# Kernel tuning notes

Hardware: AMD Instinct MI355X
Metric: run time of the kernel (lower is better)

The kernel has to match this reference:

```python
import jax, jax.numpy as jnp
import numpy as np

B, S, N, F = 4, 256, 128, 64
D = 128          # d_model == 2*F so encoder/decoder dims agree
NH = 4           # hard-coded num_heads in both MHA blocks


def _linear(x, w, b):
    # torch nn.Linear: y = x @ W.T + b, W: (out, in)
    return x @ w.T + b


def _mha(q, k, v, w_in, b_in, w_out, b_out, nh):
    # torch nn.MultiheadAttention (batch_first=True) with packed in_proj
    bq, sq, e = q.shape
    hd = e // nh
    qp = _linear(q, w_in[:e], b_in[:e])
    kp = _linear(k, w_in[e:2 * e], b_in[e:2 * e])
    vp = _linear(v, w_in[2 * e:], b_in[2 * e:])
    qh = qp.reshape(bq, sq, nh, hd)
    kh = kp.reshape(bq, k.shape[1], nh, hd)
    vh = vp.reshape(bq, v.shape[1], nh, hd)
    scores = jnp.einsum('bqhd,bkhd->bhqk', qh, kh) / np.sqrt(hd).astype(np.float32)
    attn = jax.nn.softmax(scores, axis=-1)
    out = jnp.einsum('bhqk,bkhd->bqhd', attn, vh).reshape(bq, sq, e)
    return _linear(out, w_out, b_out)


def _pos_enc(s, d):
    pos = jnp.arange(s, dtype=jnp.float32)[:, None]
    div = jnp.exp(jnp.arange(0, d, 2, dtype=jnp.float32) * (-np.log(10000.0) / d))
    pe = jnp.zeros((s, d), dtype=jnp.float32)
    pe = pe.at[:, 0::2].set(jnp.sin(pos * div))
    pe = pe.at[:, 1::2].set(jnp.cos(pos * div))
    return pe


def _haar_decouple(x):
    # exact vectorized pywt haar dwt + single-branch idwt (even seq_len)
    b, s, n, f = x.shape
    pairs = x.reshape(b, s // 2, 2, n, f)
    avg = (pairs[:, :, 0] + pairs[:, :, 1]) * 0.5  # idwt(cA, None) value
    dif = (pairs[:, :, 0] - pairs[:, :, 1]) * 0.5  # idwt(None, cD) value
    x_l = jnp.stack([avg, avg], axis=2).reshape(b, s, n, f)
    x_h = jnp.stack([dif, -dif], axis=2).reshape(b, s, n, f)
    return x_l, x_h


def setup_inputs() -> dict:
    key = jax.random.key(0)
    ks = jax.random.split(key, 32)
    p = lambda i, shp: jax.random.normal(ks[i], shp, jnp.float32) * 0.02
    return {
        'x': jax.random.normal(ks[0], (B, S, N, F), jnp.float32),
        'ts': jax.random.randint(ks[1], (B, S), 0, 252),
        'ta_w_in': p(2, (3 * D, D)), 'ta_b_in': p(3, (3 * D,)),
        'ta_w_out': p(4, (D, D)), 'ta_b_out': p(5, (D,)),
        'conv_w': p(6, (D, 2 * F, 3)), 'conv_b': p(7, (D,)),
        'pl_w': p(8, (D, D)), 'pl_b': p(9, (D,)),
        'ph_w': p(10, (D, D)), 'ph_b': p(11, (D,)),
        'as_w_in': p(12, (3 * D, D)), 'as_b_in': p(13, (3 * D,)),
        'as_w_out': p(14, (D, D)), 'as_b_out': p(15, (D,)),
        'ac_w_in': p(16, (3 * D, D)), 'ac_b_in': p(17, (3 * D,)),
        'ac_w_out': p(18, (D, D)), 'ac_b_out': p(19, (D,)),
        'rl_w': p(20, (1, D)), 'rl_b': p(21, (1,)),
        'cl_w': p(22, (2, D)), 'cl_b': p(23, (2,)),
        'rf_w': p(24, (1, D)), 'rf_b': p(25, (1,)),
        'cf_w': p(26, (2, D)), 'cf_b': p(27, (2,)),
    }


def reference(x, ts, ta_w_in, ta_b_in, ta_w_out, ta_b_out, conv_w, conv_b,
              pl_w, pl_b, ph_w, ph_b, as_w_in, as_b_in, as_w_out, as_b_out,
              ac_w_in, ac_b_in, ac_w_out, ac_b_out, rl_w, rl_b, cl_w, cl_b,
              rf_w, rf_b, cf_w, cf_b):
    b, s, n, f = x.shape
    # --- DecouplingFlowLayer (vectorized haar) ---
    x_l, x_h = _haar_decouple(x)
    xl_cat = jnp.concatenate([x, x_l], axis=-1)  # (b,s,n,2f)
    xh_cat = jnp.concatenate([x, x_h], axis=-1)
    e = 2 * f
    # --- DualFrequencyEncoder ---
    pe = _pos_enc(s, e)
    xl_flat = xl_cat.transpose(0, 2, 1, 3).reshape(b * n, s, e) + pe
    x_tatt = _mha(xl_flat, xl_flat, xl_flat, ta_w_in, ta_b_in, ta_w_out, ta_b_out, NH)
    x_l_gat = x_tatt.reshape(b, s, n, e)  # faithful raw .view() as in torch
    xh_flat = xh_cat.transpose(0, 2, 3, 1).reshape(b * n, e, s)
    conv = jax.lax.conv_general_dilated(
        xh_flat, conv_w, window_strides=(1,), padding=[(2, 2)],
        rhs_dilation=(2,), dimension_numbers=('NCH', 'OIH', 'NCH'))
    conv = jax.nn.relu(conv + conv_b[None, :, None])
    x_h_gat = conv.reshape(b, n, -1, s).transpose(0, 3, 1, 2)  # (b,s,n,D)
    d = x_h_gat.shape[-1]
    # ts -> time_embedding is computed then discarded in the original forward: dead code
    # --- DualFrequencyFusionDecoder ---
    y_l = x_l_gat.reshape(b * n, s, d)
    y_h = x_h_gat.reshape(b * n, s, d)
    q_l = _linear(y_l, pl_w, pl_b)
    k_h = _linear(y_h, ph_w, ph_b)
    y_l2 = _linear(q_l, pl_w, pl_b)  # predictor_l applied twice, as in torch
    lreg = _linear(y_l2, rl_w, rl_b).reshape(b, s, n)
    lcla = jax.nn.softmax(_linear(y_l2, cl_w, cl_b), axis=-1).reshape(b, s, n, 2)
    a_self = _mha(q_l, q_l, q_l, as_w_in, as_b_in, as_w_out, as_b_out, NH)
    a_cross = _mha(q_l, k_h, k_h, ac_w_in, ac_b_in, ac_w_out, ac_b_out, NH)
    fused = (a_self + a_cross).reshape(b, s, n, d)
    reg = _linear(fused, rf_w, rf_b)[..., 0]
    cla = jax.nn.softmax(_linear(fused, cf_w, cf_b), axis=-1)
    return reg, cla, lreg, lcla
```

## Files before the change

kernel.cpp:

```cpp
#include <hip/hip_runtime.h>
#include <hip/hip_bf16.h>

typedef __attribute__((ext_vector_type(8))) short short8v;
typedef __attribute__((ext_vector_type(4))) short short4v;
typedef __attribute__((ext_vector_type(4))) float f32x4;
typedef __hip_bfloat16 bh;

constexpr long SF_ELEMS = 131072L * 128;
#define MFMA16(a, b, c) __builtin_amdgcn_mfma_f32_16x16x32_bf16((a), (b), (c), 0, 0, 0)

__device__ __forceinline__ short bh_bits(float x) {
  bh h = __float2bfloat16(x);
  return *reinterpret_cast<short*>(&h);
}


__global__ __launch_bounds__(256) void sf_wcvt(const float* __restrict__ s0, const float* __restrict__ s1,
                                               const float* __restrict__ s2, const float* __restrict__ s3,
                                               const float* __restrict__ s4, const float* __restrict__ s5,
                                               const float* __restrict__ s6, const float* __restrict__ s7,
                                               const float* __restrict__ cw,
                                               bh* __restrict__ dst) {
  int i = blockIdx.x * 256 + threadIdx.x;
  float v;
  if      (i <  49152) v = s0[i];
  else if (i <  65536) v = s1[i - 49152];
  else if (i <  81920) v = s2[i - 65536];
  else if (i <  98304) v = s3[i - 81920];
  else if (i < 147456) v = s4[i - 98304];
  else if (i < 163840) v = s5[i - 147456];
  else if (i < 212992) v = s6[i - 163840];
  else if (i < 229376) v = s7[i - 212992];
  else if (i < 278528) {
    int j = i - 229376;
    int tap = j >> 14, rem = j & 16383;
    v = cw[rem * 3 + tap];
  } else return;
  dst[i] = __float2bfloat16(v);
}

__global__ __launch_bounds__(256) void sf_pe(float* __restrict__ pe) {
  int i = blockIdx.x * 256 + threadIdx.x;
  int e = i & 127, s = i >> 7;
  int ii = e >> 1;
  float dv = expf(-0.0719557945041855f * (float)(2 * ii));
  float ang = (float)s * dv;
  pe[i] = (e & 1) ? cosf(ang) : sinf(ang);
}

__global__ __launch_bounds__(256) void sf_buildzx(const float* __restrict__ x,
                                                  const float* __restrict__ pe,
                                                  bh* __restrict__ z,
                                                  bh* __restrict__ xh) {
  long i = (long)blockIdx.x * 256 + threadIdx.x;
  if (i >= SF_ELEMS) return;
  int e = (int)(i & 127);
  int s = (int)((i >> 7) & 255);
  int r = (int)(i >> 15);
  int b = r >> 7, stk = r & 127;
  float zv, hv;
  if (e < 64) {
    float val = x[(((long)b * 256 + s) * 128 + stk) * 64 + e];
    zv = val; hv = val;
  } else {
    int f = e - 64;
    int t2 = s >> 1;
    float a0 = x[(((long)b * 256 + 2 * t2) * 128 + stk) * 64 + f];
    float a1 = x[(((long)b * 256 + 2 * t2 + 1) * 128 + stk) * 64 + f];
    zv = 0.5f * (a0 + a1);
    float d = 0.5f * (a0 - a1);
    hv = (s & 1) ? -d : d;
  }
  z[i] = __float2bfloat16(zv + pe[s * 128 + e]);
  xh[i] = __float2bfloat16(hv);
}

__global__ __launch_bounds__(256) void sf_lin(const bh* __restrict__ X,
                                              const bh* __restrict__ Wb,
                                              const float* __restrict__ bias,
                                              bh* __restrict__ Y) {
  __shared__ bh Lw[4][32][140];
  const int t = threadIdx.x, lane = t & 63, w = t >> 6;
  const int lr = lane & 15, lg = lane >> 4;
  const long R0 = (long)blockIdx.x * 128 + w * 32;
  const f32x4 z4 = {0.f, 0.f, 0.f, 0.f};
  short8v a[2][4];
#pragma unroll
  for (int ks = 0; ks < 4; ++ks) {
    a[0][ks] = *reinterpret_cast<const short8v*>(X + (R0 + lr) * 128 + ks * 32 + lg * 8);
    a[1][ks] = *reinterpret_cast<const short8v*>(X + (R0 + 16 + lr) * 128 + ks * 32 + lg * 8);
  }
  f32x4 acc[2][8];
#pragma unroll
  for (int m = 0; m < 2; ++m)
#pragma unroll
    for (int n = 0; n < 8; ++n) acc[m][n] = z4;
#pragma unroll
  for (int ks = 0; ks < 4; ++ks) {
#pragma unroll
    for (int n = 0; n < 8; ++n) {
      short8v b = *reinterpret_cast<const short8v*>(Wb + (long)(n * 16 + lr) * 128 + ks * 32 + lg * 8);
      acc[0][n] = MFMA16(a[0][ks], b, acc[0][n]);
      acc[1][n] = MFMA16(a[1][ks], b, acc[1][n]);
    }
  }
#pragma unroll
  for (int n = 0; n < 8; ++n) {
    float bv = bias[n * 16 + lr];
#pragma unroll
    for (int m = 0; m < 2; ++m)
#pragma unroll
      for (int r = 0; r < 4; ++r)
        Lw[w][m * 16 + 4 * lg + r][n * 16 + lr] = __float2bfloat16(acc[m][n][r] + bv);
  }
#pragma unroll
  for (int c = 0; c < 8; ++c) {
    int row_l = c * 4 + lg;
    short8v v = *reinterpret_cast<const short8v*>(&Lw[w][row_l][lr * 8]);
    *reinterpret_cast<short8v*>(Y + (R0 + row_l) * 128 + lr * 8) = v;
  }
}

__global__ __launch_bounds__(256) void sf_convm(const bh* __restrict__ Xh,
                                                const bh* __restrict__ Wr,
                                                const float* __restrict__ bias,
                                                bh* __restrict__ Yh) {
  __shared__ bh Lw[4][32][140];
  const int t = threadIdx.x, lane = t & 63, w = t >> 6;
  const int lr = lane & 15, lg = lane >> 4;
  const int bnc = blockIdx.x >> 1;
  const int half = blockIdx.x & 1;
  const int b = bnc >> 7, stk = bnc & 127;
  const int R0 = half * 128 + w * 32;
  const f32x4 z4 = {0.f, 0.f, 0.f, 0.f};
  const short8v zf = {0, 0, 0, 0, 0, 0, 0, 0};
  f32x4 acc[2][8];
#pragma unroll
  for (int m = 0; m < 2; ++m)
#pragma unroll
    for (int n = 0; n < 8; ++n) acc[m][n] = z4;
#pragma unroll
  for (int tap = 0; tap < 3; ++tap) {
    const int shift = 2 * tap - 2;
#pragma unroll
    for (int ks = 0; ks < 4; ++ks) {
      int s0 = R0 + lr + shift;
      int s1 = s0 + 16;
      short8v a0 = zf, a1 = zf;
      if ((unsigned)s0 < 256u)
        a0 = *reinterpret_cast<const short8v*>(Xh + ((long)bnc * 256 + s0) * 128 + ks * 32 + lg * 8);
      if ((unsigned)s1 < 256u)
        a1 = *reinterpret_cast<const short8v*>(Xh + ((long)bnc * 256 + s1) * 128 + ks * 32 + lg * 8);
#pragma unroll
      for (int n = 0; n < 8; ++n) {
        short8v bb = *reinterpret_cast<const short8v*>(Wr + (long)tap * 16384 + (long)(n * 16 + lr) * 128 + ks * 32 + lg * 8);
        acc[0][n] = MFMA16(a0, bb, acc[0][n]);
        acc[1][n] = MFMA16(a1, bb, acc[1][n]);
      }
    }
  }
#pragma unroll
  for (int n = 0; n < 8; ++n) {
    float bv = bias[n * 16 + lr];
#pragma unroll
    for (int m = 0; m < 2; ++m)
#pragma unroll
      for (int r = 0; r < 4; ++r)
        Lw[w][m * 16 + 4 * lg + r][n * 16 + lr] = __float2bfloat16(fmaxf(acc[m][n][r] + bv, 0.f));
  }
#pragma unroll
  for (int c = 0; c < 8; ++c) {
    int row_l = c * 4 + lg;
    int sc = R0 + row_l;
    int rp = b * 128 + (sc >> 1);
    int sp = ((sc & 1) << 7) + stk;
    short8v v = *reinterpret_cast<const short8v*>(&Lw[w][row_l][lr * 8]);
    *reinterpret_cast<short8v*>(Yh + ((long)rp * 256 + sp) * 128 + lr * 8) = v;
  }
}

__global__ __launch_bounds__(256) void sf_attnp(const bh* Qsrc, const bh* KVsrc,
                                                const bh* __restrict__ Win,
                                                const float* __restrict__ bin,
                                                bh* __restrict__ O) {
  __shared__ bh Ks[256][36];
  __shared__ bh Vt[32][260];
  __shared__ bh QP[4][64][36];
  const int t = threadIdx.x, lane = t & 63, w = t >> 6;
  const int lr = lane & 15, lg = lane >> 4;
  const int bn = blockIdx.x >> 2, h = blockIdx.x & 3;
  const long R0 = (long)bn * 256;
  const int ch = h * 32;
  const f32x4 z4 = {0.f, 0.f, 0.f, 0.f};
  const float SC2 = 0.2550351f;
  {
    short8v wq[2][4];
#pragma unroll
    for (int n = 0; n < 2; ++n)
#pragma unroll
      for (int ks = 0; ks < 4; ++ks)
        wq[n][ks] = *reinterpret_cast<const short8v*>(Win + (long)(ch + n * 16 + lr) * 128 + ks * 32 + lg * 8);
#pragma unroll
    for (int m2 = 0; m2 < 4; ++m2) {
      short8v asv[4];
#pragma unroll
      for (int ks = 0; ks < 4; ++ks)
        asv[ks] = *reinterpret_cast<const short8v*>(Qsrc + (R0 + w * 64 + m2 * 16 + lr) * 128 + ks * 32 + lg * 8);
#pragma unroll
      for (int n = 0; n < 2; ++n) {
        f32x4 acc = z4;
#pragma unroll
        for (int ks = 0; ks < 4; ++ks) acc = MFMA16(asv[ks], wq[n][ks], acc);
        float bb = bin[ch + n * 16 + lr];
#pragma unroll
        for (int r = 0; r < 4; ++r)
          QP[w][m2 * 16 + 4 * lg + r][n * 16 + lr] = __float2bfloat16((acc[r] + bb) * SC2);
      }
    }
  }
  {
    short8v wk[2][4], wv[2][4];
#pragma unroll
    for (int n = 0; n < 2; ++n)
#pragma unroll
      for (int ks = 0; ks < 4; ++ks) {
        wk[n][ks] = *reinterpret_cast<const short8v*>(Win + (long)(128 + ch + n * 16 + lr) * 128 + ks * 32 + lg * 8);
        wv[n][ks] = *reinterpret_cast<const short8v*>(Win + (long)(256 + ch + n * 16 + lr) * 128 + ks * 32 + lg * 8);
      }
#pragma unroll
    for (int m2 = 0; m2 < 4; ++m2) {
      short8v asv[4];
#pragma unroll
      for (int ks = 0; ks < 4; ++ks)
        asv[ks] = *reinterpret_cast<const short8v*>(KVsrc + (R0 + w * 64 + m2 * 16 + lr) * 128 + ks * 32 + lg * 8);
#pragma unroll
      for (int n = 0; n < 2; ++n) {
        f32x4 ak = z4, av = z4;
#pragma unroll
        for (int ks = 0; ks < 4; ++ks) {
          ak = MFMA16(asv[ks], wk[n][ks], ak);
          av = MFMA16(asv[ks], wv[n][ks], av);
        }
        float bk = bin[128 + ch + n * 16 + lr];
        float bv = bin[256 + ch + n * 16 + lr];
#pragma unroll
        for (int r = 0; r < 4; ++r)
          Ks[w * 64 + m2 * 16 + 4 * lg + r][n * 16 + lr] = __float2bfloat16(ak[r] + bk);
        short4v pv;
#pragma unroll
        for (int r = 0; r < 4; ++r) pv[r] = bh_bits(av[r] + bv);
        *reinterpret_cast<short4v*>(&Vt[n * 16 + lr][w * 64 + m2 * 16 + 4 * lg]) = pv;
      }
    }
  }
  __syncthreads();
  short8v aq[4];
#pragma unroll
  for (int mt = 0; mt < 4; ++mt)
    aq[mt] = *reinterpret_cast<const short8v*>(&QP[w][mt * 16 + lr][lg * 8]);
  bh* plp = &QP[w][0][0];
  f32x4 Oacc[4][2];
  float psum[4] = {0.f, 0.f, 0.f, 0.f};
#pragma unroll
  for (int mt = 0; mt < 4; ++mt) { Oacc[mt][0] = z4; Oacc[mt][1] = z4; }
#pragma unroll
  for (int kt = 0; kt < 4; ++kt) {
    short8v bvf[2][2];
#pragma unroll
    for (int dt = 0; dt < 2; ++dt)
#pragma unroll
      for (int ks = 0; ks < 2; ++ks)
        bvf[dt][ks] = *reinterpret_cast<const short8v*>(&Vt[dt * 16 + lr][kt * 64 + ks * 32 + lg * 8]);
#pragma unroll
    for (int mt = 0; mt < 4; ++mt) {
      f32x4 st[4];
#pragma unroll
      for (int nt = 0; nt < 4; ++nt) {
        short8v bk = *reinterpret_cast<const short8v*>(&Ks[kt * 64 + nt * 16 + lr][lg * 8]);
        st[nt] = MFMA16(bk, aq[mt], z4);
      }
      float ps = 0.f;
#pragma unroll
      for (int nt = 0; nt < 4; ++nt) {
        float p0 = exp2f(st[nt][0]);
        float p1 = exp2f(st[nt][1]);
        float p2 = exp2f(st[nt][2]);
        float p3 = exp2f(st[nt][3]);
        ps += (p0 + p1) + (p2 + p3);
        short4v pk;
        pk[0] = bh_bits(p0); pk[1] = bh_bits(p1); pk[2] = bh_bits(p2); pk[3] = bh_bits(p3);
        *reinterpret_cast<short4v*>(&plp[lr * 72 + nt * 16 + 4 * lg]) = pk;
      }
      psum[mt] += ps;
#pragma unroll
      for (int ks = 0; ks < 2; ++ks) {
        short8v ap = *reinterpret_cast<const short8v*>(&plp[lr * 72 + ks * 32 + lg * 8]);
        Oacc[mt][0] = MFMA16(ap, bvf[0][ks], Oacc[mt][0]);
        Oacc[mt][1] = MFMA16(ap, bvf[1][ks], Oacc[mt][1]);
      }
    }
  }
#pragma unroll
  for (int mt = 0; mt < 4; ++mt) {
    float ps = psum[mt];
    ps += __shfl_xor(ps, 16, 64);
    ps += __shfl_xor(ps, 32, 64);
    float inv = 1.f / ps;
#pragma unroll
    for (int r = 0; r < 4; ++r) {
      float invr = __shfl(inv, 4 * lg + r, 64);
      long row = R0 + w * 64 + mt * 16 + 4 * lg + r;
      O[row * 128 + ch + lr]      = __float2bfloat16(Oacc[mt][0][r] * invr);
      O[row * 128 + ch + 16 + lr] = __float2bfloat16(Oacc[mt][1][r] * invr);
    }
  }
}

__global__ __launch_bounds__(256) void sf_encdec(const bh* __restrict__ X,
                                                 const bh* __restrict__ Wo, const float* __restrict__ bo,
                                                 const bh* __restrict__ Wpl, const float* __restrict__ bpl,
                                                 const float* __restrict__ rw, const float* __restrict__ rb,
                                                 const float* __restrict__ cw, const float* __restrict__ cb,
                                                 bh* __restrict__ Yq, float* __restrict__ out,
                                                 long off_reg, long off_cla) {
  __shared__ bh Lw[4][32][140];
  __shared__ float hw[3][128];
  const int t = threadIdx.x, lane = t & 63, w = t >> 6;
  const int lr = lane & 15, lg = lane >> 4;
  const long R0 = (long)blockIdx.x * 128 + w * 32;
  const f32x4 z4 = {0.f, 0.f, 0.f, 0.f};
  if (t < 128) { hw[0][t] = rw[t]; hw[1][t] = cw[t]; hw[2][t] = cw[128 + t]; }
  {
    short8v a[2][4];
#pragma unroll
    for (int ks = 0; ks < 4; ++ks) {
      a[0][ks] = *reinterpret_cast<const short8v*>(X + (R0 + lr) * 128 + ks * 32 + lg * 8);
      a[1][ks] = *reinterpret_cast<const short8v*>(X + (R0 + 16 + lr) * 128 + ks * 32 + lg * 8);
    }
    f32x4 acc[2][8];
#pragma unroll
    for (int m = 0; m < 2; ++m)
#pragma unroll
      for (int n = 0; n < 8; ++n) acc[m][n] = z4;
#pragma unroll
    for (int ks = 0; ks < 4; ++ks)
#pragma unroll
      for (int n = 0; n < 8; ++n) {
        short8v b = *reinterpret_cast<const short8v*>(Wo + (long)(n * 16 + lr) * 128 + ks * 32 + lg * 8);
        acc[0][n] = MFMA16(a[0][ks], b, acc[0][n]);
        acc[1][n] = MFMA16(a[1][ks], b, acc[1][n]);
      }
#pragma unroll
    for (int n = 0; n < 8; ++n) {
      float bv = bo[n * 16 + lr];
#pragma unroll
      for (int m = 0; m < 2; ++m)
#pragma unroll
        for (int r = 0; r < 4; ++r)
          Lw[w][m * 16 + 4 * lg + r][n * 16 + lr] = __float2bfloat16(acc[m][n][r] + bv);
    }
  }
#pragma unroll
  for (int stage = 0; stage < 2; ++stage) {
    short8v a[2][4];
#pragma unroll
    for (int ks = 0; ks < 4; ++ks) {
      a[0][ks] = *reinterpret_cast<const short8v*>(&Lw[w][lr][ks * 32 + lg * 8]);
      a[1][ks] = *reinterpret_cast<const short8v*>(&Lw[w][16 + lr][ks * 32 + lg * 8]);
    }
    f32x4 acc[2][8];
#pragma unroll
    for (int m = 0; m < 2; ++m)
#pragma unroll
      for (int n = 0; n < 8; ++n) acc[m][n] = z4;
#pragma unroll
    for (int ks = 0; ks < 4; ++ks)
#pragma unroll
      for (int n = 0; n < 8; ++n) {
        short8v b = *reinterpret_cast<const short8v*>(Wpl + (long)(n * 16 + lr) * 128 + ks * 32 + lg * 8);
        acc[0][n] = MFMA16(a[0][ks], b, acc[0][n]);
        acc[1][n] = MFMA16(a[1][ks], b, acc[1][n]);
      }
#pragma unroll
    for (int n = 0; n < 8; ++n) {
      float bv = bpl[n * 16 + lr];
#pragma unroll
      for (int m = 0; m < 2; ++m)
#pragma unroll
        for (int r = 0; r < 4; ++r)
          Lw[w][m * 16 + 4 * lg + r][n * 16 + lr] = __float2bfloat16(acc[m][n][r] + bv);
    }
    if (stage == 0) {
#pragma unroll
      for (int c = 0; c < 8; ++c) {
        int row_l = c * 4 + lg;
        short8v v = *reinterpret_cast<const short8v*>(&Lw[w][row_l][lr * 8]);
        *reinterpret_cast<short8v*>(Yq + (R0 + row_l) * 128 + lr * 8) = v;
      }
    }
  }
  __syncthreads();
  {
    const int rr = lane >> 1, hh = lane & 1;
    float d0 = 0.f, d1 = 0.f, d2 = 0.f;
#pragma unroll
    for (int j = 0; j < 8; ++j) {
      short8v v8 = *reinterpret_cast<const short8v*>(&Lw[w][rr][hh * 64 + j * 8]);
      const bh* vv = reinterpret_cast<const bh*>(&v8);
#pragma unroll
      for (int k = 0; k < 8; ++k) {
        float f = __bfloat162float(vv[k]);
        int c = hh * 64 + j * 8 + k;
        d0 = fmaf(f, hw[0][c], d0);
        d1 = fmaf(f, hw[1][c], d1);
        d2 = fmaf(f, hw[2][c], d2);
      }
    }
    d0 += __shfl_xor(d0, 1, 64);
    d1 += __shfl_xor(d1, 1, 64);
    d2 += __shfl_xor(d2, 1, 64);
    if (hh == 0) {
      long row = R0 + rr;
      d0 += rb[0]; d1 += cb[0]; d2 += cb[1];
      float mx = fmaxf(d1, d2);
      float e1 = __expf(d1 - mx), e2 = __expf(d2 - mx);
      float inv = 1.f / (e1 + e2);
      out[off_reg + row] = d0;
      out[off_cla + row * 2] = e1 * inv;
      out[off_cla + row * 2 + 1] = e2 * inv;
    }
  }
}

__global__ __launch_bounds__(256) void sf_fin(const bh* __restrict__ X,
                                              const bh* __restrict__ Was, const float* __restrict__ bo,
                                              const bh* __restrict__ Prev,
                                              const float* __restrict__ rw, const float* __restrict__ rb,
                                              const float* __restrict__ cw, const float* __restrict__ cb,
                                              float* __restrict__ out, long off_reg, long off_cla) {
  __shared__ bh Lw[4][32][140];
  __shared__ float hw[3][128];
  const int t = threadIdx.x, lane = t & 63, w = t >> 6;
  const int lr = lane & 15, lg = lane >> 4;
  const long R0 = (long)blockIdx.x * 128 + w * 32;
  const f32x4 z4 = {0.f, 0.f, 0.f, 0.f};
  if (t < 128) { hw[0][t] = rw[t]; hw[1][t] = cw[t]; hw[2][t] = cw[128 + t]; }
  {
    short8v a[2][4];
#pragma unroll
    for (int ks = 0; ks < 4; ++ks) {
      a[0][ks] = *reinterpret_cast<const short8v*>(X + (R0 + lr) * 128 + ks * 32 + lg * 8);
      a[1][ks] = *reinterpret_cast<const short8v*>(X + (R0 + 16 + lr) * 128 + ks * 32 + lg * 8);
    }
    f32x4 acc[2][8];
#pragma unroll
    for (int m = 0; m < 2; ++m)
#pragma unroll
      for (int n = 0; n < 8; ++n) acc[m][n] = z4;
#pragma unroll
    for (int ks = 0; ks < 4; ++ks)
#pragma unroll
      for (int n = 0; n < 8; ++n) {
        short8v b = *reinterpret_cast<const short8v*>(Was + (long)(n * 16 + lr) * 128 + ks * 32 + lg * 8);
        acc[0][n] = MFMA16(a[0][ks], b, acc[0][n]);
        acc[1][n] = MFMA16(a[1][ks], b, acc[1][n]);
      }
#pragma unroll
    for (int n = 0; n < 8; ++n) {
      float bv = bo[n * 16 + lr];
#pragma unroll
      for (int m = 0; m < 2; ++m)
#pragma unroll
        for (int r = 0; r < 4; ++r)
          Lw[w][m * 16 + 4 * lg + r][n * 16 + lr] = __float2bfloat16(acc[m][n][r] + bv);
    }
  }
  __syncthreads();
  {
    const int rr = lane >> 1, hh = lane & 1;
    float d0 = 0.f, d1 = 0.f, d2 = 0.f;
#pragma unroll
    for (int j = 0; j < 8; ++j) {
      short8v v8 = *reinterpret_cast<const short8v*>(&Lw[w][rr][hh * 64 + j * 8]);
      short8v p8 = *reinterpret_cast<const short8v*>(Prev + (R0 + rr) * 128 + hh * 64 + j * 8);
      const bh* vv = reinterpret_cast<const bh*>(&v8);
      const bh* pp = reinterpret_cast<const bh*>(&p8);
#pragma unroll
      for (int k = 0; k < 8; ++k) {
        float f = __bfloat162float(vv[k]) + __bfloat162float(pp[k]);
        int c = hh * 64 + j * 8 + k;
        d0 = fmaf(f, hw[0][c], d0);
        d1 = fmaf(f, hw[1][c], d1);
        d2 = fmaf(f, hw[2][c], d2);
      }
    }
    d0 += __shfl_xor(d0, 1, 64);
    d1 += __shfl_xor(d1, 1, 64);
    d2 += __shfl_xor(d2, 1, 64);
    if (hh == 0) {
      long row = R0 + rr;
      d0 += rb[0]; d1 += cb[0]; d2 += cb[1];
      float mx = fmaxf(d1, d2);
      float e1 = __expf(d1 - mx), e2 = __expf(d2 - mx);
      float inv = 1.f / (e1 + e2);
      out[off_reg + row] = d0;
      out[off_cla + row * 2] = e1 * inv;
      out[off_cla + row * 2 + 1] = e2 * inv;
    }
  }
}

extern "C" void kernel_launch(void* const* d_in, const int* in_sizes, int n_in,
                              void* d_out, int out_size, void* d_ws, size_t ws_size,
                              hipStream_t stream) {
  (void)in_sizes; (void)n_in; (void)out_size; (void)ws_size;
  const float* x       = (const float*)d_in[0];
  const float* ta_w_in = (const float*)d_in[2];
  const float* ta_b_in = (const float*)d_in[3];
  const float* ta_w_o  = (const float*)d_in[4];
  const float* ta_b_o  = (const float*)d_in[5];
  const float* conv_w  = (const float*)d_in[6];
  const float* conv_b  = (const float*)d_in[7];
  const float* pl_w    = (const float*)d_in[8];
  const float* pl_b    = (const float*)d_in[9];
  const float* ph_w    = (const float*)d_in[10];
  const float* ph_b    = (const float*)d_in[11];
  const float* as_w_in = (const float*)d_in[12];
  const float* as_b_in = (const float*)d_in[13];
  const float* as_w_o  = (const float*)d_in[14];
  const float* as_b_o  = (const float*)d_in[15];
  const float* ac_w_in = (const float*)d_in[16];
  const float* ac_b_in = (const float*)d_in[17];
  const float* ac_w_o  = (const float*)d_in[18];
  const float* ac_b_o  = (const float*)d_in[19];
  const float* rl_w    = (const float*)d_in[20];
  const float* rl_b    = (const float*)d_in[21];
  const float* cl_w    = (const float*)d_in[22];
  const float* cl_b    = (const float*)d_in[23];
  const float* rf_w    = (const float*)d_in[24];
  const float* rf_b    = (const float*)d_in[25];
  const float* cf_w    = (const float*)d_in[26];
  const float* cf_b    = (const float*)d_in[27];
  float* out = (float*)d_out;

  bh* S0 = (bh*)d_ws;
  bh* S1 = S0 + SF_ELEMS;
  bh* S2 = S1 + SF_ELEMS;
  bh* S3 = S2 + SF_ELEMS;
  bh* S4 = S3 + SF_ELEMS;
  bh* A  = S4 + SF_ELEMS;
  float* PE = (float*)(A + 278528);

  dim3 blk(256);
  const int GZ = (int)(SF_ELEMS / 256);
  const int GL = 1024;

  sf_wcvt<<<1088, blk, 0, stream>>>(ta_w_in, ta_w_o, pl_w, ph_w, ac_w_in, ac_w_o,
                                    as_w_in, as_w_o, conv_w, A);
  sf_pe<<<128, blk, 0, stream>>>(PE);

  sf_buildzx<<<GZ, blk, 0, stream>>>(x, PE, S0, S3);
  sf_attnp<<<2048, blk, 0, stream>>>(S0, S0, A, ta_b_in, S1);
  sf_encdec<<<GL, blk, 0, stream>>>(S1, A + 49152, ta_b_o, A + 65536, pl_b,
                                    rl_w, rl_b, cl_w, cl_b, S2, out,
                                    393216L, 524288L);
  sf_convm<<<1024, blk, 0, stream>>>(S3, A + 229376, conv_b, S4);
  sf_lin<<<GL, blk, 0, stream>>>(S4, A + 81920, ph_b, S0);

  sf_attnp<<<2048, blk, 0, stream>>>(S2, S0, A + 98304, ac_b_in, S3);
  sf_lin<<<GL, blk, 0, stream>>>(S3, A + 147456, ac_b_o, S4);

  sf_attnp<<<2048, blk, 0, stream>>>(S2, S2, A + 163840, as_b_in, S1);
  sf_fin<<<GL, blk, 0, stream>>>(S1, A + 212992, as_b_o, S4,
                                 rf_w, rf_b, cf_w, cf_b, out, 0L, 131072L);
}
```

Before: 471.2 us.

## Merge independent decoder stages into combined launches and fuse output projections

Folds positional-encoding generation into the weight-conversion kernel. Runs the encoder-output/predictor chain and the conv+predictor_h chain in one launch, split by block index. Runs the cross- and self-attention kernels together in a single launch. Fuses both attention output projections into the final head kernel by summing the two GEMMs in one accumulator. The aim is fewer launches, fewer intermediate round trips through global memory, and better GPU fill; the cost is larger kernels that may use more registers, with uneven work across the blocks of a merged launch.

Measured after the change: 479.3 us. Within noise of the previous version (+1.7%).

```diff
diff --git a/kernel.cpp b/kernel.cpp
--- a/kernel.cpp
+++ b/kernel.cpp
@@ -20,8 +20,19 @@
                                                const float* __restrict__ s4, const float* __restrict__ s5,
                                                const float* __restrict__ s6, const float* __restrict__ s7,
                                                const float* __restrict__ cw,
-                                               bh* __restrict__ dst) {
+                                               bh* __restrict__ dst, float* __restrict__ pe) {
   int i = blockIdx.x * 256 + threadIdx.x;
+  if (i >= 278528) {
+    int j = i - 278528;
+    if (j < 32768) {
+      int e = j & 127, s = j >> 7;
+      int ii = e >> 1;
+      float dv = expf(-0.0719557945041855f * (float)(2 * ii));
+      float ang = (float)s * dv;
+      pe[j] = (e & 1) ? cosf(ang) : sinf(ang);
+    }
+    return;
+  }
   float v;
   if      (i <  49152) v = s0[i];
   else if (i <  65536) v = s1[i - 49152];
@@ -31,21 +42,12 @@
   else if (i < 163840) v = s5[i - 147456];
   else if (i < 212992) v = s6[i - 163840];
   else if (i < 229376) v = s7[i - 212992];
-  else if (i < 278528) {
+  else {
     int j = i - 229376;
     int tap = j >> 14, rem = j & 16383;
     v = cw[rem * 3 + tap];
-  } else return;
+  }
   dst[i] = __float2bfloat16(v);
-}
-
-__global__ __launch_bounds__(256) void sf_pe(float* __restrict__ pe) {
-  int i = blockIdx.x * 256 + threadIdx.x;
-  int e = i & 127, s = i >> 7;
-  int ii = e >> 1;
-  float dv = expf(-0.0719557945041855f * (float)(2 * ii));
-  float ang = (float)s * dv;
-  pe[i] = (e & 1) ? cosf(ang) : sinf(ang);
 }
 
 __global__ __launch_bounds__(256) void sf_buildzx(const float* __restrict__ x,
@@ -75,125 +77,21 @@
   xh[i] = __float2bfloat16(hv);
 }
 
-__global__ __launch_bounds__(256) void sf_lin(const bh* __restrict__ X,
-                                              const bh* __restrict__ Wb,
-                                              const float* __restrict__ bias,
-                                              bh* __restrict__ Y) {
-  __shared__ bh Lw[4][32][140];
+__device__ __forceinline__ void attn_body(const bh* Qsrc, const bh* KVsrc,
+                                          const bh* __restrict__ Win,
+                                          const float* __restrict__ bin,
+                                          bh* __restrict__ O, int bn, int h,
+                                          bh (*Ks)[36], bh (*Vt)[260],
+                                          bh (*Pl)[2][16][72]) {
   const int t = threadIdx.x, lane = t & 63, w = t >> 6;
   const int lr = lane & 15, lg = lane >> 4;
-  const long R0 = (long)blockIdx.x * 128 + w * 32;
-  const f32x4 z4 = {0.f, 0.f, 0.f, 0.f};
-  short8v a[2][4];
-#pragma unroll
-  for (int ks = 0; ks < 4; ++ks) {
-    a[0][ks] = *reinterpret_cast<const short8v*>(X + (R0 + lr) * 128 + ks * 32 + lg * 8);
-    a[1][ks] = *reinterpret_cast<const short8v*>(X + (R0 + 16 + lr) * 128 + ks * 32 + lg * 8);
-  }
-  f32x4 acc[2][8];
-#pragma unroll
-  for (int m = 0; m < 2; ++m)
-#pragma unroll
-    for (int n = 0; n < 8; ++n) acc[m][n] = z4;
-#pragma unroll
-  for (int ks = 0; ks < 4; ++ks) {
-#pragma unroll
-    for (int n = 0; n < 8; ++n) {
-      short8v b = *reinterpret_cast<const short8v*>(Wb + (long)(n * 16 + lr) * 128 + ks * 32 + lg * 8);
-      acc[0][n] = MFMA16(a[0][ks], b, acc[0][n]);
-      acc[1][n] = MFMA16(a[1][ks], b, acc[1][n]);
-    }
-  }
-#pragma unroll
-  for (int n = 0; n < 8; ++n) {
-    float bv = bias[n * 16 + lr];
-#pragma unroll
-    for (int m = 0; m < 2; ++m)
-#pragma unroll
-      for (int r = 0; r < 4; ++r)
-        Lw[w][m * 16 + 4 * lg + r][n * 16 + lr] = __float2bfloat16(acc[m][n][r] + bv);
-  }
-#pragma unroll
-  for (int c = 0; c < 8; ++c) {
-    int row_l = c * 4 + lg;
-    short8v v = *reinterpret_cast<const short8v*>(&Lw[w][row_l][lr * 8]);
-    *reinterpret_cast<short8v*>(Y + (R0 + row_l) * 128 + lr * 8) = v;
-  }
-}
-
-__global__ __launch_bounds__(256) void sf_convm(const bh* __restrict__ Xh,
-                                                const bh* __restrict__ Wr,
-                                                const float* __restrict__ bias,
-                                                bh* __restrict__ Yh) {
-  __shared__ bh Lw[4][32][140];
-  const int t = threadIdx.x, lane = t & 63, w = t >> 6;
-  const int lr = lane & 15, lg = lane >> 4;
-  const int bnc = blockIdx.x >> 1;
-  const int half = blockIdx.x & 1;
-  const int b = bnc >> 7, stk = bnc & 127;
-  const int R0 = half * 128 + w * 32;
-  const f32x4 z4 = {0.f, 0.f, 0.f, 0.f};
-  const short8v zf = {0, 0, 0, 0, 0, 0, 0, 0};
-  f32x4 acc[2][8];
-#pragma unroll
-  for (int m = 0; m < 2; ++m)
-#pragma unroll
-    for (int n = 0; n < 8; ++n) acc[m][n] = z4;
-#pragma unroll
-  for (int tap = 0; tap < 3; ++tap) {
-    const int shift = 2 * tap - 2;
-#pragma unroll
-    for (int ks = 0; ks < 4; ++ks) {
-      int s0 = R0 + lr + shift;
-      int s1 = s0 + 16;
-      short8v a0 = zf, a1 = zf;
-      if ((unsigned)s0 < 256u)
-        a0 = *reinterpret_cast<const short8v*>(Xh + ((long)bnc * 256 + s0) * 128 + ks * 32 + lg * 8);
-      if ((unsigned)s1 < 256u)
-        a1 = *reinterpret_cast<const short8v*>(Xh + ((long)bnc * 256 + s1) * 128 + ks * 32 + lg * 8);
-#pragma unroll
-      for (int n = 0; n < 8; ++n) {
-        short8v bb = *reinterpret_cast<const short8v*>(Wr + (long)tap * 16384 + (long)(n * 16 + lr) * 128 + ks * 32 + lg * 8);
-        acc[0][n] = MFMA16(a0, bb, acc[0][n]);
-        acc[1][n] = MFMA16(a1, bb, acc[1][n]);
-      }
-    }
-  }
-#pragma unroll
-  for (int n = 0; n < 8; ++n) {
-    float bv = bias[n * 16 + lr];
-#pragma unroll
-    for (int m = 0; m < 2; ++m)
-#pragma unroll
-      for (int r = 0; r < 4; ++r)
-        Lw[w][m * 16 + 4 * lg + r][n * 16 + lr] = __float2bfloat16(fmaxf(acc[m][n][r] + bv, 0.f));
-  }
-#pragma unroll
-  for (int c = 0; c < 8; ++c) {
-    int row_l = c * 4 + lg;
-    int sc = R0 + row_l;
-    int rp = b * 128 + (sc >> 1);
-    int sp = ((sc & 1) << 7) + stk;
-    short8v v = *reinterpret_cast<const short8v*>(&Lw[w][row_l][lr * 8]);
-    *reinterpret_cast<short8v*>(Yh + ((long)rp * 256 + sp) * 128 + lr * 8) = v;
-  }
-}
-
-__global__ __launch_bounds__(256) void sf_attnp(const bh* Qsrc, const bh* KVsrc,
-                                                const bh* __restrict__ Win,
-                                                const float* __restrict__ bin,
-                                                bh* __restrict__ O) {
-  __shared__ bh Ks[256][36];
-  __shared__ bh Vt[32][260];
-  __shared__ bh QP[4][64][36];
-  const int t = threadIdx.x, lane = t & 63, w = t >> 6;
-  const int lr = lane & 15, lg = lane >> 4;
-  const int bn = blockIdx.x >> 2, h = blockIdx.x & 3;
   const long R0 = (long)bn * 256;
   const int ch = h * 32;
   const f32x4 z4 = {0.f, 0.f, 0.f, 0.f};
   const float SC2 = 0.2550351f;
+  short8v aq[4];
   {
+    bh* scr = &Pl[w][0][0][0];
     short8v wq[2][4];
 #pragma unroll
     for (int n = 0; n < 2; ++n)
@@ -214,8 +112,9 @@
         float bb = bin[ch + n * 16 + lr];
 #pragma unroll
         for (int r = 0; r < 4; ++r)
-          QP[w][m2 * 16 + 4 * lg + r][n * 16 + lr] = __float2bfloat16((acc[r] + bb) * SC2);
-      }
+          scr[(4 * lg + r) * 72 + n * 16 + lr] = __float2bfloat16((acc[r] + bb) * SC2);
+      }
+      aq[m2] = *reinterpret_cast<const short8v*>(&scr[lr * 72 + lg * 8]);
     }
   }
   {
@@ -254,11 +153,6 @@
     }
   }
   __syncthreads();
-  short8v aq[4];
-#pragma unroll
-  for (int mt = 0; mt < 4; ++mt)
-    aq[mt] = *reinterpret_cast<const short8v*>(&QP[w][mt * 16 + lr][lg * 8]);
-  bh* plp = &QP[w][0][0];
   f32x4 Oacc[4][2];
   float psum[4] = {0.f, 0.f, 0.f, 0.f};
 #pragma unroll
@@ -273,6 +167,7 @@
         bvf[dt][ks] = *reinterpret_cast<const short8v*>(&Vt[dt * 16 + lr][kt * 64 + ks * 32 + lg * 8]);
 #pragma unroll
     for (int mt = 0; mt < 4; ++mt) {
+      bh* plp = &Pl[w][mt & 1][0][0];
       f32x4 st[4];
 #pragma unroll
       for (int nt = 0; nt < 4; ++nt) {
@@ -316,13 +211,243 @@
   }
 }
 
-__global__ __launch_bounds__(256) void sf_encdec(const bh* __restrict__ X,
-                                                 const bh* __restrict__ Wo, const float* __restrict__ bo,
-                                                 const bh* __restrict__ Wpl, const float* __restrict__ bpl,
-                                                 const float* __restrict__ rw, const float* __restrict__ rb,
-                                                 const float* __restrict__ cw, const float* __restrict__ cb,
-                                                 bh* __restrict__ Yq, float* __restrict__ out,
-                                                 long off_reg, long off_cla) {
+__global__ __launch_bounds__(256) void sf_attnp(const bh* Qsrc, const bh* KVsrc,
+                                                const bh* __restrict__ Win,
+                                                const float* __restrict__ bin,
+                                                bh* __restrict__ O) {
+  __shared__ bh Ks[256][36];
+  __shared__ bh Vt[32][260];
+  __shared__ bh Pl[4][2][16][72];
+  attn_body(Qsrc, KVsrc, Win, bin, O, blockIdx.x >> 2, blockIdx.x & 3, Ks, Vt, Pl);
+}
+
+__global__ __launch_bounds__(256) void sf_attnp2(const bh* Qc, const bh* KVc,
+                                                 const bh* __restrict__ Wc, const float* __restrict__ bc,
+                                                 bh* __restrict__ Oc,
+                                                 const bh* Qs, const bh* KVs,
+                                                 const bh* __restrict__ Wsl, const float* __restrict__ bsl,
+                                                 bh* __restrict__ Os) {
+  __shared__ bh Ks[256][36];
+  __shared__ bh Vt[32][260];
+  __shared__ bh Pl[4][2][16][72];
+  int g = blockIdx.x;
+  if (g < 2048)
+    attn_body(Qc, KVc, Wc, bc, Oc, g >> 2, g & 3, Ks, Vt, Pl);
+  else {
+    g -= 2048;
+    attn_body(Qs, KVs, Wsl, bsl, Os, g >> 2, g & 3, Ks, Vt, Pl);
+  }
+}
+
+__global__ __launch_bounds__(256) void sf_dec(const bh* __restrict__ X,
+                                              const bh* __restrict__ Wo, const float* __restrict__ bo,
+                                              const bh* __restrict__ Wpl, const float* __restrict__ bpl,
+                                              const float* __restrict__ rw, const float* __restrict__ rb,
+                                              const float* __restrict__ cw, const float* __restrict__ cb,
+                                              bh* __restrict__ Yq, float* __restrict__ out,
+                                              long off_reg, long off_cla,
+                                              const bh* __restrict__ Xh,
+                                              const bh* __restrict__ Wr, const float* __restrict__ cbias,
+                                              const bh* __restrict__ Wph, const float* __restrict__ bph,
+                                              bh* __restrict__ KH) {
+  __shared__ bh Lw[4][32][140];
+  __shared__ float hw[3][128];
+  const int t = threadIdx.x, lane = t & 63, w = t >> 6;
+  const int lr = lane & 15, lg = lane >> 4;
+  const f32x4 z4 = {0.f, 0.f, 0.f, 0.f};
+  if (blockIdx.x < 1024) {
+    const long R0 = (long)blockIdx.x * 128 + w * 32;
+    if (t < 128) { hw[0][t] = rw[t]; hw[1][t] = cw[t]; hw[2][t] = cw[128 + t]; }
+    {
+      short8v a[2][4];
+#pragma unroll
+      for (int ks = 0; ks < 4; ++ks) {
+        a[0][ks] = *reinterpret_cast<const short8v*>(X + (R0 + lr) * 128 + ks * 32 + lg * 8);
+        a[1][ks] = *reinterpret_cast<const short8v*>(X + (R0 + 16 + lr) * 128 + ks * 32 + lg * 8);
+      }
+      f32x4 acc[2][8];
+#pragma unroll
+      for (int m = 0; m < 2; ++m)
+#pragma unroll
+        for (int n = 0; n < 8; ++n) acc[m][n] = z4;
+#pragma unroll
+      for (int ks = 0; ks < 4; ++ks)
+#pragma unroll
+        for (int n = 0; n < 8; ++n) {
+          short8v b = *reinterpret_cast<const short8v*>(Wo + (long)(n * 16 + lr) * 128 + ks * 32 + lg * 8);
+          acc[0][n] = MFMA16(a[0][ks], b, acc[0][n]);
+          acc[1][n] = MFMA16(a[1][ks], b, acc[1][n]);
+        }
+#pragma unroll
+      for (int n = 0; n < 8; ++n) {
+        float bv = bo[n * 16 + lr];
+#pragma unroll
+        for (int m = 0; m < 2; ++m)
+#pragma unroll
+          for (int r = 0; r < 4; ++r)
+            Lw[w][m * 16 + 4 * lg + r][n * 16 + lr] = __float2bfloat16(acc[m][n][r] + bv);
+      }
+    }
+#pragma unroll
+    for (int stage = 0; stage < 2; ++stage) {
+      short8v a[2][4];
+#pragma unroll
+      for (int ks = 0; ks < 4; ++ks) {
+        a[0][ks] = *reinterpret_cast<const short8v*>(&Lw[w][lr][ks * 32 + lg * 8]);
+        a[1][ks] = *reinterpret_cast<const short8v*>(&Lw[w][16 + lr][ks * 32 + lg * 8]);
+      }
+      f32x4 acc[2][8];
+#pragma unroll
+      for (int m = 0; m < 2; ++m)
+#pragma unroll
+        for (int n = 0; n < 8; ++n) acc[m][n] = z4;
+#pragma unroll
+      for (int ks = 0; ks < 4; ++ks)
+#pragma unroll
+        for (int n = 0; n < 8; ++n) {
+          short8v b = *reinterpret_cast<const short8v*>(Wpl + (long)(n * 16 + lr) * 128 + ks * 32 + lg * 8);
+          acc[0][n] = MFMA16(a[0][ks], b, acc[0][n]);
+          acc[1][n] = MFMA16(a[1][ks], b, acc[1][n]);
+        }
+#pragma unroll
+      for (int n = 0; n < 8; ++n) {
+        float bv = bpl[n * 16 + lr];
+#pragma unroll
+        for (int m = 0; m < 2; ++m)
+#pragma unroll
+          for (int r = 0; r < 4; ++r)
+            Lw[w][m * 16 + 4 * lg + r][n * 16 + lr] = __float2bfloat16(acc[m][n][r] + bv);
+      }
+      if (stage == 0) {
+#pragma unroll
+        for (int c = 0; c < 8; ++c) {
+          int row_l = c * 4 + lg;
+          short8v v = *reinterpret_cast<const short8v*>(&Lw[w][row_l][lr * 8]);
+          *reinterpret_cast<short8v*>(Yq + (R0 + row_l) * 128 + lr * 8) = v;
+        }
+      }
+    }
+    __syncthreads();
+    {
+      const int rr = lane >> 1, hh = lane & 1;
+      float d0 = 0.f, d1 = 0.f, d2 = 0.f;
+#pragma unroll
+      for (int j = 0; j < 8; ++j) {
+        short8v v8 = *reinterpret_cast<const short8v*>(&Lw[w][rr][hh * 64 + j * 8]);
+        const bh* vv = reinterpret_cast<const bh*>(&v8);
+#pragma unroll
+        for (int k = 0; k < 8; ++k) {
+          float f = __bfloat162float(vv[k]);
+          int c = hh * 64 + j * 8 + k;
+          d0 = fmaf(f, hw[0][c], d0);
+          d1 = fmaf(f, hw[1][c], d1);
+          d2 = fmaf(f, hw[2][c], d2);
+        }
+      }
+      d0 += __shfl_xor(d0, 1, 64);
+      d1 += __shfl_xor(d1, 1, 64);
+      d2 += __shfl_xor(d2, 1, 64);
+      if (hh == 0) {
+        long row = R0 + rr;
+        d0 += rb[0]; d1 += cb[0]; d2 += cb[1];
+        float mx = fmaxf(d1, d2);
+        float e1 = __expf(d1 - mx), e2 = __expf(d2 - mx);
+        float inv = 1.f / (e1 + e2);
+        out[off_reg + row] = d0;
+        out[off_cla + row * 2] = e1 * inv;
+        out[off_cla + row * 2 + 1] = e2 * inv;
+      }
+    }
+  } else {
+    int bid = blockIdx.x - 1024;
+    const int bnc = bid >> 1;
+    const int half = bid & 1;
+    const int b = bnc >> 7, stk = bnc & 127;
+    const int R0 = half * 128 + w * 32;
+    const short8v zf = {0, 0, 0, 0, 0, 0, 0, 0};
+    f32x4 acc[2][8];
+#pragma unroll
+    for (int m = 0; m < 2; ++m)
+#pragma unroll
+      for (int n = 0; n < 8; ++n) acc[m][n] = z4;
+#pragma unroll
+    for (int tap = 0; tap < 3; ++tap) {
+      const int shift = 2 * tap - 2;
+#pragma unroll
+      for (int ks = 0; ks < 4; ++ks) {
+        int s0 = R0 + lr + shift;
+        int s1 = s0 + 16;
+        short8v a0 = zf, a1 = zf;
+        if ((unsigned)s0 < 256u)
+          a0 = *reinterpret_cast<const short8v*>(Xh + ((long)bnc * 256 + s0) * 128 + ks * 32 + lg * 8);
+        if ((unsigned)s1 < 256u)
+          a1 = *reinterpret_cast<const short8v*>(Xh + ((long)bnc * 256 + s1) * 128 + ks * 32 + lg * 8);
+#pragma unroll
+        for (int n = 0; n < 8; ++n) {
+          short8v bb = *reinterpret_cast<const short8v*>(Wr + (long)tap * 16384 + (long)(n * 16 + lr) * 128 + ks * 32 + lg * 8);
+          acc[0][n] = MFMA16(a0, bb, acc[0][n]);
+          acc[1][n] = MFMA16(a1, bb, acc[1][n]);
+        }
+      }
+    }
+#pragma unroll
+    for (int n = 0; n < 8; ++n) {
+      float bv = cbias[n * 16 + lr];
+#pragma unroll
+      for (int m = 0; m < 2; ++m)
+#pragma unroll
+        for (int r = 0; r < 4; ++r)
+          Lw[w][m * 16 + 4 * lg + r][n * 16 + lr] = __float2bfloat16(fmaxf(acc[m][n][r] + bv, 0.f));
+    }
+    {
+      short8v a2[2][4];
+#pragma unroll
+      for (int ks = 0; ks < 4; ++ks) {
+        a2[0][ks] = *reinterpret_cast<const short8v*>(&Lw[w][lr][ks * 32 + lg * 8]);
+        a2[1][ks] = *reinterpret_cast<const short8v*>(&Lw[w][16 + lr][ks * 32 + lg * 8]);
+      }
+      f32x4 ac2[2][8];
+#pragma unroll
+      for (int m = 0; m < 2; ++m)
+#pragma unroll
+        for (int n = 0; n < 8; ++n) ac2[m][n] = z4;
+#pragma unroll
+      for (int ks = 0; ks < 4; ++ks)
+#pragma unroll
+        for (int n = 0; n < 8; ++n) {
+          short8v b2 = *reinterpret_cast<const short8v*>(Wph + (long)(n * 16 + lr) * 128 + ks * 32 + lg * 8);
+          ac2[0][n] = MFMA16(a2[0][ks], b2, ac2[0][n]);
+          ac2[1][n] = MFMA16(a2[1][ks], b2, ac2[1][n]);
+        }
+#pragma unroll
+      for (int n = 0; n < 8; ++n) {
+        float bv = bph[n * 16 + lr];
+#pragma unroll
+        for (int m = 0; m < 2; ++m)
+#pragma unroll
+          for (int r = 0; r < 4; ++r)
+            Lw[w][m * 16 + 4 * lg + r][n * 16 + lr] = __float2bfloat16(ac2[m][n][r] + bv);
+      }
+    }
+#pragma unroll
+    for (int c = 0; c < 8; ++c) {
+      int row_l = c * 4 + lg;
+      int sc = R0 + row_l;
+      int rp = b * 128 + (sc >> 1);
+      int sp = ((sc & 1) << 7) + stk;
+      short8v v = *reinterpret_cast<const short8v*>(&Lw[w][row_l][lr * 8]);
+      *reinterpret_cast<short8v*>(KH + ((long)rp * 256 + sp) * 128 + lr * 8) = v;
+    }
+  }
+}
+
+__global__ __launch_bounds__(256) void sf_fin2(const bh* __restrict__ Xs,
+                                               const bh* __restrict__ Was, const float* __restrict__ bs,
+                                               const bh* __restrict__ Xc,
+                                               const bh* __restrict__ Wac, const float* __restrict__ bc,
+                                               const float* __restrict__ rw, const float* __restrict__ rb,
+                                               const float* __restrict__ cw, const float* __restrict__ cb,
+                                               float* __restrict__ out, long off_reg, long off_cla) {
   __shared__ bh Lw[4][32][140];
   __shared__ float hw[3][128];
   const int t = threadIdx.x, lane = t & 63, w = t >> 6;
@@ -331,72 +456,51 @@
   const f32x4 z4 = {0.f, 0.f, 0.f, 0.f};
   if (t < 128) { hw[0][t] = rw[t]; hw[1][t] = cw[t]; hw[2][t] = cw[128 + t]; }
   {
-    short8v a[2][4];
-#pragma unroll
-    for (int ks = 0; ks < 4; ++ks) {
-      a[0][ks] = *reinterpret_cast<const short8v*>(X + (R0 + lr) * 128 + ks * 32 + lg * 8);
-      a[1][ks] = *reinterpret_cast<const short8v*>(X + (R0 + 16 + lr) * 128 + ks * 32 + lg * 8);
-    }
     f32x4 acc[2][8];
 #pragma unroll
     for (int m = 0; m < 2; ++m)
 #pragma unroll
       for (int n = 0; n < 8; ++n) acc[m][n] = z4;
-#pragma unroll
-    for (int ks = 0; ks < 4; ++ks)
-#pragma unroll
-      for (int n = 0; n < 8; ++n) {
-        short8v b = *reinterpret_cast<const short8v*>(Wo + (long)(n * 16 + lr) * 128 + ks * 32 + lg * 8);
-        acc[0][n] = MFMA16(a[0][ks], b, acc[0][n]);
-        acc[1][n] = MFMA16(a[1][ks], b, acc[1][n]);
-      }
+    {
+      short8v a[2][4];
+#pragma unroll
+      for (int ks = 0; ks < 4; ++ks) {
+        a[0][ks] = *reinterpret_cast<const short8v*>(Xs + (R0 + lr) * 128 + ks * 32 + lg * 8);
+        a[1][ks] = *reinterpret_cast<const short8v*>(Xs + (R0 + 16 + lr) * 128 + ks * 32 + lg * 8);
+      }
+#pragma unroll
+      for (int ks = 0; ks < 4; ++ks)
+#pragma unroll
+        for (int n = 0; n < 8; ++n) {
+          short8v b = *reinterpret_cast<const short8v*>(Was + (long)(n * 16 + lr) * 128 + ks * 32 + lg * 8);
+          acc[0][n] = MFMA16(a[0][ks], b, acc[0][n]);
+          acc[1][n] = MFMA16(a[1][ks], b, acc[1][n]);
+        }
+    }
+    {
+      short8v a[2][4];
+#pragma unroll
+      for (int ks = 0; ks < 4; ++ks) {
+        a[0][ks] = *reinterpret_cast<const short8v*>(Xc + (R0 + lr) * 128 + ks * 32 + lg * 8);
+        a[1][ks] = *reinterpret_cast<const short8v*>(Xc + (R0 + 16 + lr) * 128 + ks * 32 + lg * 8);
+      }
+#pragma unroll
+      for (int ks = 0; ks < 4; ++ks)
+#pragma unroll
+        for (int n = 0; n < 8; ++n) {
+          short8v b = *reinterpret_cast<const short8v*>(Wac + (long)(n * 16 + lr) * 128 + ks * 32 + lg * 8);
+          acc[0][n] = MFMA16(a[0][ks], b, acc[0][n]);
+          acc[1][n] = MFMA16(a[1][ks], b, acc[1][n]);
+        }
+    }
 #pragma unroll
     for (int n = 0; n < 8; ++n) {
-      float bv = bo[n * 16 + lr];
+      float bv = bs[n * 16 + lr] + bc[n * 16 + lr];
 #pragma unroll
       for (int m = 0; m < 2; ++m)
 #pragma unroll
         for (int r = 0; r < 4; ++r)
           Lw[w][m * 16 + 4 * lg + r][n * 16 + lr] = __float2bfloat16(acc[m][n][r] + bv);
-    }
-  }
-#pragma unroll
-  for (int stage = 0; stage < 2; ++stage) {
-    short8v a[2][4];
-#pragma unroll
-    for (int ks = 0; ks < 4; ++ks) {
-      a[0][ks] = *reinterpret_cast<const short8v*>(&Lw[w][lr][ks * 32 + lg * 8]);
-      a[1][ks] = *reinterpret_cast<const short8v*>(&Lw[w][16 + lr][ks * 32 + lg * 8]);
-    }
-    f32x4 acc[2][8];
-#pragma unroll
-    for (int m = 0; m < 2; ++m)
-#pragma unroll
-      for (int n = 0; n < 8; ++n) acc[m][n] = z4;
-#pragma unroll
-    for (int ks = 0; ks < 4; ++ks)
-#pragma unroll
-      for (int n = 0; n < 8; ++n) {
-        short8v b = *reinterpret_cast<const short8v*>(Wpl + (long)(n * 16 + lr) * 128 + ks * 32 + lg * 8);
-        acc[0][n] = MFMA16(a[0][ks], b, acc[0][n]);
-        acc[1][n] = MFMA16(a[1][ks], b, acc[1][n]);
-      }
-#pragma unroll
-    for (int n = 0; n < 8; ++n) {
-      float bv = bpl[n * 16 + lr];
-#pragma unroll
-      for (int m = 0; m < 2; ++m)
-#pragma unroll
-        for (int r = 0; r < 4; ++r)
-          Lw[w][m * 16 + 4 * lg + r][n * 16 + lr] = __float2bfloat16(acc[m][n][r] + bv);
-    }
-    if (stage == 0) {
-#pragma unroll
-      for (int c = 0; c < 8; ++c) {
-        int row_l = c * 4 + lg;
-        short8v v = *reinterpret_cast<const short8v*>(&Lw[w][row_l][lr * 8]);
-        *reinterpret_cast<short8v*>(Yq + (R0 + row_l) * 128 + lr * 8) = v;
-      }
     }
   }
   __syncthreads();
@@ -410,84 +514,6 @@
 #pragma unroll
       for (int k = 0; k < 8; ++k) {
         float f = __bfloat162float(vv[k]);
-        int c = hh * 64 + j * 8 + k;
-        d0 = fmaf(f, hw[0][c], d0);
-        d1 = fmaf(f, hw[1][c], d1);
-        d2 = fmaf(f, hw[2][c], d2);
-      }
-    }
-    d0 += __shfl_xor(d0, 1, 64);
-    d1 += __shfl_xor(d1, 1, 64);
-    d2 += __shfl_xor(d2, 1, 64);
-    if (hh == 0) {
-      long row = R0 + rr;
-      d0 += rb[0]; d1 += cb[0]; d2 += cb[1];
-      float mx = fmaxf(d1, d2);
-      float e1 = __expf(d1 - mx), e2 = __expf(d2 - mx);
-      float inv = 1.f / (e1 + e2);
-      out[off_reg + row] = d0;
-      out[off_cla + row * 2] = e1 * inv;
-      out[off_cla + row * 2 + 1] = e2 * inv;
-    }
-  }
-}
-
-__global__ __launch_bounds__(256) void sf_fin(const bh* __restrict__ X,
-                                              const bh* __restrict__ Was, const float* __restrict__ bo,
-                                              const bh* __restrict__ Prev,
-                                              const float* __restrict__ rw, const float* __restrict__ rb,
-                                              const float* __restrict__ cw, const float* __restrict__ cb,
-                                              float* __restrict__ out, long off_reg, long off_cla) {
-  __shared__ bh Lw[4][32][140];
-  __shared__ float hw[3][128];
-  const int t = threadIdx.x, lane = t & 63, w = t >> 6;
-  const int lr = lane & 15, lg = lane >> 4;
-  const long R0 = (long)blockIdx.x * 128 + w * 32;
-  const f32x4 z4 = {0.f, 0.f, 0.f, 0.f};
-  if (t < 128) { hw[0][t] = rw[t]; hw[1][t] = cw[t]; hw[2][t] = cw[128 + t]; }
-  {
-    short8v a[2][4];
-#pragma unroll
-    for (int ks = 0; ks < 4; ++ks) {
-      a[0][ks] = *reinterpret_cast<const short8v*>(X + (R0 + lr) * 128 + ks * 32 + lg * 8);
-      a[1][ks] = *reinterpret_cast<const short8v*>(X + (R0 + 16 + lr) * 128 + ks * 32 + lg * 8);
-    }
-    f32x4 acc[2][8];
-#pragma unroll
-    for (int m = 0; m < 2; ++m)
-#pragma unroll
-      for (int n = 0; n < 8; ++n) acc[m][n] = z4;
-#pragma unroll
-    for (int ks = 0; ks < 4; ++ks)
-#pragma unroll
-      for (int n = 0; n < 8; ++n) {
-        short8v b = *reinterpret_cast<const short8v*>(Was + (long)(n * 16 + lr) * 128 + ks * 32 + lg * 8);
-        acc[0][n] = MFMA16(a[0][ks], b, acc[0][n]);
-        acc[1][n] = MFMA16(a[1][ks], b, acc[1][n]);
-      }
-#pragma unroll
-    for (int n = 0; n < 8; ++n) {
-      float bv = bo[n * 16 + lr];
-#pragma unroll
-      for (int m = 0; m < 2; ++m)
-#pragma unroll
-        for (int r = 0; r < 4; ++r)
-          Lw[w][m * 16 + 4 * lg + r][n * 16 + lr] = __float2bfloat16(acc[m][n][r] + bv);
-    }
-  }
-  __syncthreads();
-  {
-    const int rr = lane >> 1, hh = lane & 1;
-    float d0 = 0.f, d1 = 0.f, d2 = 0.f;
-#pragma unroll
-    for (int j = 0; j < 8; ++j) {
-      short8v v8 = *reinterpret_cast<const short8v*>(&Lw[w][rr][hh * 64 + j * 8]);
-      short8v p8 = *reinterpret_cast<const short8v*>(Prev + (R0 + rr) * 128 + hh * 64 + j * 8);
-      const bh* vv = reinterpret_cast<const bh*>(&v8);
-      const bh* pp = reinterpret_cast<const bh*>(&p8);
-#pragma unroll
-      for (int k = 0; k < 8; ++k) {
-        float f = __bfloat162float(vv[k]) + __bfloat162float(pp[k]);
         int c = hh * 64 + j * 8 + k;
         d0 = fmaf(f, hw[0][c], d0);
         d1 = fmaf(f, hw[1][c], d1);
@@ -553,24 +579,16 @@
 
   dim3 blk(256);
   const int GZ = (int)(SF_ELEMS / 256);
-  const int GL = 1024;
-
-  sf_wcvt<<<1088, blk, 0, stream>>>(ta_w_in, ta_w_o, pl_w, ph_w, ac_w_in, ac_w_o,
-                                    as_w_in, as_w_o, conv_w, A);
-  sf_pe<<<128, blk, 0, stream>>>(PE);
-
+
+  sf_wcvt<<<1216, blk, 0, stream>>>(ta_w_in, ta_w_o, pl_w, ph_w, ac_w_in, ac_w_o,
+                                    as_w_in, as_w_o, conv_w, A, PE);
   sf_buildzx<<<GZ, blk, 0, stream>>>(x, PE, S0, S3);
   sf_attnp<<<2048, blk, 0, stream>>>(S0, S0, A, ta_b_in, S1);
-  sf_encdec<<<GL, blk, 0, stream>>>(S1, A + 49152, ta_b_o, A + 65536, pl_b,
-                                    rl_w, rl_b, cl_w, cl_b, S2, out,
-                                    393216L, 524288L);
-  sf_convm<<<1024, blk, 0, stream>>>(S3, A + 229376, conv_b, S4);
-  sf_lin<<<GL, blk, 0, stream>>>(S4, A + 81920, ph_b, S0);
-
-  sf_attnp<<<2048, blk, 0, stream>>>(S2, S0, A + 98304, ac_b_in, S3);
-  sf_lin<<<GL, blk, 0, stream>>>(S3, A + 147456, ac_b_o, S4);
-
-  sf_attnp<<<2048, blk, 0, stream>>>(S2, S2, A + 163840, as_b_in, S1);
-  sf_fin<<<GL, blk, 0, stream>>>(S1, A + 212992, as_b_o, S4,
-                                 rf_w, rf_b, cf_w, cf_b, out, 0L, 131072L);
-}
+  sf_dec<<<2048, blk, 0, stream>>>(S1, A + 49152, ta_b_o, A + 65536, pl_b,
+                                   rl_w, rl_b, cl_w, cl_b, S2, out, 393216L, 524288L,
+                                   S3, A + 229376, conv_b, A + 81920, ph_b, S4);
+  sf_attnp2<<<4096, blk, 0, stream>>>(S2, S4, A + 98304, ac_b_in, S0,
+                                      S2, S2, A + 163840, as_b_in, S3);
+  sf_fin2<<<1024, blk, 0, stream>>>(S3, A + 212992, as_b_o, S0, A + 147456, ac_b_o,
+                                    rf_w, rf_b, cf_w, cf_b, out, 0L, 131072L);
+}
```
